# Kernel optimization log

Hardware: AMD Instinct MI355X
Metric: run time of the kernel (lower is better)

## Reference

```python
import jax, jax.numpy as jnp
import numpy as np
from jax import lax

TOP_N = 4
CAT_NUM = 4
IOU_THRESH = 0.25
PAD = 224
OUT_SZ = 224


def _gen_edge_anchors():
    # Faithful port of NTSNet._generate_default_anchor_maps for 448x448 input.
    settings = (
        dict(stride=32, size=48, scale=[2 ** (1.0 / 3.0), 2 ** (2.0 / 3.0)], ar=[0.667, 1, 1.5]),
        dict(stride=64, size=96, scale=[2 ** (1.0 / 3.0), 2 ** (2.0 / 3.0)], ar=[0.667, 1, 1.5]),
        dict(stride=128, size=192, scale=[1, 2 ** (1.0 / 3.0), 2 ** (2.0 / 3.0)], ar=[0.667, 1, 1.5]),
    )
    inp = np.array([448, 448], dtype=np.float32)
    edges = []
    for s in settings:
        stride = s['stride']
        oh, ow = np.ceil(inp / stride).astype(int)
        ostart = stride / 2.0
        oy = np.arange(ostart, ostart + stride * oh, stride, dtype=np.float32).reshape(oh, 1)
        ox = np.arange(ostart, ostart + stride * ow, stride, dtype=np.float32).reshape(1, ow)
        cy = np.broadcast_to(oy, (oh, ow)); cx = np.broadcast_to(ox, (oh, ow))
        for sc in s['scale']:
            for ar in s['ar']:
                h = s['size'] * sc / float(ar) ** 0.5
                w = s['size'] * sc * float(ar) ** 0.5
                e = np.stack([cy - h / 2.0, cx - w / 2.0, cy + h / 2.0, cx + w / 2.0], axis=-1).reshape(-1, 4)
                edges.append(e)
    return np.concatenate(edges, 0).astype(np.float32)

EDGE_ANCHORS = (_gen_edge_anchors() + PAD).astype(np.int32)  # [1614,4] (y0,x0,y1,x1) in padded coords
BOXES_F = jnp.asarray(EDGE_ANCHORS, jnp.float32)
BOXES_I = jnp.asarray(EDGE_ANCHORS, jnp.int32)
AREAS = (BOXES_F[:, 2] - BOXES_F[:, 0]) * (BOXES_F[:, 3] - BOXES_F[:, 1])
N_ANCHORS = EDGE_ANCHORS.shape[0]  # 1614


def _nms_single(scores):
    # Greedy hard NMS: pick top score, suppress IoU >= thresh, repeat TOP_N times.
    def step(valid, _):
        s = jnp.where(valid, scores, -jnp.inf)
        i = jnp.argmax(s)
        b = BOXES_F[i]
        sy = jnp.maximum(BOXES_F[:, 0], b[0]); sx = jnp.maximum(BOXES_F[:, 1], b[1])
        ey = jnp.minimum(BOXES_F[:, 2], b[2]); ex = jnp.minimum(BOXES_F[:, 3], b[3])
        ly = ey - sy; lx = ex - sx
        inter = jnp.where((ly < 0) | (lx < 0), 0.0, ly * lx)
        iou = inter / (AREAS + AREAS[i] - inter)
        return valid & (iou < IOU_THRESH), i
    _, idx = lax.scan(step, jnp.ones((N_ANCHORS,), bool), None, length=TOP_N)
    return idx  # [TOP_N] int


def _crop_resize(img, box):
    # img: [3, 896, 896]; box: int [4] = (y0,x0,y1,x1); bilinear, align_corners=True -> [3,224,224]
    hmax = img.shape[-1] - 1
    y0, x0, y1, x1 = box[0], box[1], box[2], box[3]
    t = jnp.arange(OUT_SZ, dtype=jnp.float32) / (OUT_SZ - 1.0)
    ys = y0.astype(jnp.float32) + t * (y1 - y0 - 1).astype(jnp.float32)
    xs = x0.astype(jnp.float32) + t * (x1 - x0 - 1).astype(jnp.float32)
    yf = jnp.floor(ys); xf = jnp.floor(xs)
    wy = (ys - yf)[None, :, None]; wx = (xs - xf)[None, None, :]
    yl = yf.astype(jnp.int32); yh = jnp.minimum(yl + 1, hmax)
    xl = xf.astype(jnp.int32); xh = jnp.minimum(xl + 1, hmax)
    g = lambda yi, xi: img[:, yi[:, None], xi[None, :]]
    top = g(yl, xl) * (1.0 - wx) + g(yl, xh) * wx
    bot = g(yh, xl) * (1.0 - wx) + g(yh, xh) * wx
    return top * (1.0 - wy) + bot * wy


def _conv(x, w, b, stride, pad):
    y = lax.conv_general_dilated(x, w, (stride, stride), ((pad, pad), (pad, pad)),
                                 dimension_numbers=('NCHW', 'OIHW', 'NCHW'))
    return y + b[None, :, None, None]


def _forward(x, bb_w, bb_b, w1, b1, t1w, t1b, w2, b2, t2w, t2b, w3, b3, t3w, t3b, cw, cb):
    B = x.shape[0]
    backbone = lambda z: jax.nn.relu(_conv(z, bb_w, bb_b, 32, 0))
    raw_pre = backbone(x)  # [B,2048,14,14]
    # Navigator unit
    y1 = jax.nn.relu(_conv(raw_pre, w1, b1, 1, 1))                                  # [B,128,14,14]
    z1 = (jnp.einsum('bchw,oc->bohw', y1, t1w) + t1b[None, :, None, None]).reshape(B, -1)
    y2 = jax.nn.relu(_conv(y1, w2, b2, 2, 1))                                        # [B,128,7,7]
    z2 = (jnp.einsum('bchw,oc->bohw', y2, t2w) + t2b[None, :, None, None]).reshape(B, -1)
    y3 = jax.nn.relu(_conv(y2, w3, b3, 2, 1))                                        # [B,128,4,4]
    z3 = (jnp.einsum('bchw,oc->bohw', y3, t3w) + t3b[None, :, None, None]).reshape(B, -1)
    rpn_score = jnp.concatenate([z1, z2, z3], axis=1)  # [B,1614]
    top_idx = jax.vmap(_nms_single)(rpn_score)          # [B,TOP_N]
    boxes = BOXES_I[top_idx]                            # [B,TOP_N,4]
    x_pad = jnp.pad(x, ((0, 0), (0, 0), (PAD, PAD), (PAD, PAD)))  # [B,3,896,896]
    parts = jax.vmap(lambda img, bs: jax.vmap(lambda b: _crop_resize(img, b))(bs))(x_pad, boxes)
    parts = lax.stop_gradient(parts).reshape(B * TOP_N, 3, OUT_SZ, OUT_SZ)  # .detach() in torch
    part_feat = backbone(parts).mean(axis=(2, 3)).reshape(B, TOP_N, 2048)
    part_feat = part_feat[:, :CAT_NUM].reshape(B, -1)   # [B,8192]
    raw_feat = lax.stop_gradient(raw_pre).mean(axis=(2, 3))  # [B,2048] (detached in torch)
    concat = jnp.concatenate([part_feat, raw_feat], axis=1)  # [B,10240]
    return concat @ cw.T + cb                           # [B,200]


def setup_inputs() -> dict:
    key = jax.random.key(0)
    ks = jax.random.split(key, 12)
    def w(k, shape, fan_in):
        return jax.random.normal(k, shape, jnp.float32) * np.float32(np.sqrt(2.0 / fan_in))
    return {
        'x': jax.random.normal(ks[0], (8, 3, 448, 448), jnp.float32),
        'bb_w': w(ks[1], (2048, 3, 32, 32), 3 * 32 * 32), 'bb_b': jnp.zeros((2048,), jnp.float32),
        'w1': w(ks[2], (128, 2048, 3, 3), 2048 * 9), 'b1': jnp.zeros((128,), jnp.float32),
        't1w': w(ks[3], (6, 128), 128), 't1b': jnp.zeros((6,), jnp.float32),
        'w2': w(ks[4], (128, 128, 3, 3), 128 * 9), 'b2': jnp.zeros((128,), jnp.float32),
        't2w': w(ks[5], (6, 128), 128), 't2b': jnp.zeros((6,), jnp.float32),
        'w3': w(ks[6], (128, 128, 3, 3), 128 * 9), 'b3': jnp.zeros((128,), jnp.float32),
        't3w': w(ks[7], (9, 128), 128), 't3b': jnp.zeros((9,), jnp.float32),
        'cw': w(ks[8], (200, 2048 * (CAT_NUM + 1)), 2048 * (CAT_NUM + 1)),
        'cb': jnp.zeros((200,), jnp.float32),
    }


def reference(x, bb_w, bb_b, w1, b1, t1w, t1b, w2, b2, t2w, t2b, w3, b3, t3w, t3b, cw, cb):
    return _forward(x, bb_w, bb_b, w1, b1, t1w, t1b, w2, b2, t2w, t2b, w3, b3, t3w, t3b, cw, cb)
```

## Files before the change

kernel.cpp:

```cpp
#include <hip/hip_runtime.h>
#include <math.h>


typedef _Float16 h8 __attribute__((ext_vector_type(8)));
typedef float f32x4 __attribute__((ext_vector_type(4)));

#define ASCALE 256.0f
#define WSCALE 16384.0f
#define RSCALE (1.0f / (256.0f * 16384.0f))
#define PSLAB ((size_t)1664 * 2048)

__device__ __forceinline__ void gload16(const void* g, void* l) {
  __builtin_amdgcn_global_load_lds(
      (__attribute__((address_space(1))) void*)(void*)(uintptr_t)g,
      (__attribute__((address_space(3))) void*)l, 16, 0, 0);
}

__device__ void anchors_body(int i, int* anch, float* areas) {
  if (i >= 1614) return;
  int stride, oh, a, pos;
  double size, sc;
  const double C13 = 1.2599210498948732;
  const double C23 = 1.5874010519681994;
  if (i < 1176) {
    stride = 32; size = 48.0; oh = 14; a = i / 196; pos = i % 196;
    sc = (a / 3 == 0) ? C13 : C23;
  } else if (i < 1470) {
    int r = i - 1176; stride = 64; size = 96.0; oh = 7; a = r / 49; pos = r % 49;
    sc = (a / 3 == 0) ? C13 : C23;
  } else {
    int r = i - 1470; stride = 128; size = 192.0; oh = 4; a = r / 16; pos = r % 16;
    int si = a / 3;
    sc = (si == 0) ? 1.0 : ((si == 1) ? C13 : C23);
  }
  int ari = a % 3;
  double ar = (ari == 0) ? 0.667 : ((ari == 1) ? 1.0 : 1.5);
  int gy = pos / oh, gx = pos % oh;
  float cy = 0.5f * (float)stride + (float)(stride * gy);
  float cx = 0.5f * (float)stride + (float)(stride * gx);
  double ss = sqrt(ar);
  double hd = (size * sc) / ss;
  double wd = (size * sc) * ss;
  float hh = (float)(hd * 0.5), wh = (float)(wd * 0.5);
  int y0 = (int)((cy - hh) + 224.0f), x0 = (int)((cx - wh) + 224.0f);
  int y1i = (int)((cy + hh) + 224.0f), x1i = (int)((cx + wh) + 224.0f);
  anch[i * 4 + 0] = y0; anch[i * 4 + 1] = x0;
  anch[i * 4 + 2] = y1i; anch[i * 4 + 3] = x1i;
  areas[i] = (float)(y1i - y0) * (float)(x1i - x0);
}

__global__ __launch_bounds__(256) void prep_small(int* __restrict__ anch,
                                                  float* __restrict__ areas,
                                                  const float* __restrict__ w2,
                                                  float* __restrict__ w2p,
                                                  const float* __restrict__ w3,
                                                  float* __restrict__ w3p) {
  int b = blockIdx.x, t = threadIdx.x;
  if (b < 7) { anchors_body(b * 256 + t, anch, areas); return; }
  const float* src; float* dst; int idx;
  if (b < 7 + 576) { src = w2; dst = w2p; idx = (b - 7) * 256 + t; }
  else             { src = w3; dst = w3p; idx = (b - 583) * 256 + t; }
  if (idx >= 128 * 9 * 128) return;
  int c = idx % 128; int r2 = idx / 128; int tap = r2 % 9; int o = r2 / 9;
  dst[idx] = src[(o * 128 + c) * 9 + tap];
}

__global__ __launch_bounds__(256) void split_w(const float* __restrict__ src,
                                               _Float16* __restrict__ h,
                                               _Float16* __restrict__ l, int n8) {
  int i = blockIdx.x * 256 + threadIdx.x;
  if (i >= n8) return;
  float4 v0 = *(const float4*)(src + (size_t)i * 8);
  float4 v1 = *(const float4*)(src + (size_t)i * 8 + 4);
  float vv[8] = {v0.x, v0.y, v0.z, v0.w, v1.x, v1.y, v1.z, v1.w};
  h8 vh, vl;
#pragma unroll
  for (int j = 0; j < 8; ++j) {
    float s = vv[j] * WSCALE;
    _Float16 a = (_Float16)s;
    vh[j] = a; vl[j] = (_Float16)(s - (float)a);
  }
  *(h8*)(h + (size_t)i * 8) = vh;
  *(h8*)(l + (size_t)i * 8) = vl;
}

__global__ __launch_bounds__(256) void split_w1(const float* __restrict__ w1,
                                                _Float16* __restrict__ h,
                                                _Float16* __restrict__ l) {
  int idx = blockIdx.x * 256 + threadIdx.x;
  if (idx >= 128 * 9 * 2048) return;
  int c = idx & 2047; int rest = idx >> 11; int tap = rest % 9; int o = rest / 9;
  float v = w1[(o * 2048 + c) * 9 + tap] * WSCALE;
  _Float16 a = (_Float16)v;
  h[idx] = a; l[idx] = (_Float16)(v - (float)a);
}

__global__ __launch_bounds__(256) void split_x(const float* __restrict__ x,
                                               _Float16* __restrict__ Ah,
                                               _Float16* __restrict__ Al) {
  int i = blockIdx.x * 256 + threadIdx.x;
  if (i >= 1664 * 384) return;
  int kq = i % 384, m = i / 384;
  int k = kq * 8;
  h8 vh = {}, vl = {};
  if (m < 1568) {
    int b = m / 196, pos = m % 196;
    int c = k >> 10, r = (k >> 5) & 31, col = k & 31;
    int py = (pos / 14) * 32 + r, px = (pos % 14) * 32 + col;
    const float* sp2 = x + (((size_t)(b * 3 + c) * 448 + py) * 448 + px);
    float4 v0 = *(const float4*)sp2;
    float4 v1 = *(const float4*)(sp2 + 4);
    float vv[8] = {v0.x, v0.y, v0.z, v0.w, v1.x, v1.y, v1.z, v1.w};
#pragma unroll
    for (int j = 0; j < 8; ++j) {
      float s = vv[j] * ASCALE;
      _Float16 a = (_Float16)s;
      vh[j] = a; vl[j] = (_Float16)(s - (float)a);
    }
  }
  *(h8*)(Ah + (size_t)m * 3072 + k) = vh;
  *(h8*)(Al + (size_t)m * 3072 + k) = vl;
}

__global__ __launch_bounds__(256) void gemm_bb_mfma(
    const _Float16* __restrict__ Ah, const _Float16* __restrict__ Al,
    const _Float16* __restrict__ Bh, const _Float16* __restrict__ Bl,
    float* __restrict__ P) {
  __shared__ __align__(16) char lds[65536];
  const int t = threadIdx.x;
  const int bid = blockIdx.x + 13 * blockIdx.y;
  const int orig = (bid & 7) * 26 + (bid >> 3);
  const int m0 = (orig % 13) * 128, n0 = (orig / 13) * 128;
  const int kz = blockIdx.z;
  const int lane = t & 63, w = t >> 6;
  const int wm = (w >> 1) * 64, wn = (w & 1) * 64;
  const int lrow = lane & 15, kg = lane >> 4;

  int offA[4], offB[4];
#pragma unroll
  for (int i = 0; i < 4; ++i) {
    int ba = (wm + i * 16 + lrow) * 64 + kg * 16;
    offA[i] = ba ^ (((ba >> 7) & 3) << 4);
    int bb2 = (wn + i * 16 + lrow) * 64 + kg * 16;
    offB[i] = bb2 ^ (((bb2 >> 7) & 3) << 4);
  }
  size_t gAo[2], gBo[2];
  int ldso[2];
#pragma unroll
  for (int e = 0; e < 2; ++e) {
    int p = e * 256 + t;
    int lsl = p ^ ((p >> 3) & 3);
    int row = lsl >> 2, kq = lsl & 3;
    gAo[e] = (size_t)(m0 + row) * 3072 + kq * 8;
    gBo[e] = (size_t)(n0 + row) * 3072 + kq * 8;
    ldso[e] = e * 4096 + (t & 192) * 16;
  }

  auto STAGE = [&](int buf, int k0) {
    char* L = lds + buf * 32768;
#pragma unroll
    for (int e = 0; e < 2; ++e) {
      gload16(Ah + gAo[e] + k0, L + ldso[e]);
      gload16(Al + gAo[e] + k0, L + 8192 + ldso[e]);
      gload16(Bh + gBo[e] + k0, L + 16384 + ldso[e]);
      gload16(Bl + gBo[e] + k0, L + 24576 + ldso[e]);
    }
  };

  f32x4 acc[4][4] = {};
  const int kbeg = kz * 1536, kend = kbeg + 1536;
  STAGE(0, kbeg);
  __syncthreads();
  int cur = 0;
  for (int k0 = kbeg; k0 < kend; k0 += 32) {
    if (k0 + 32 < kend) STAGE(cur ^ 1, k0 + 32);
    const char* L = lds + cur * 32768;
    h8 fah[4], fal[4], fbh[4], fbl[4];
#pragma unroll
    for (int i = 0; i < 4; ++i) {
      fah[i] = *(const h8*)(L + offA[i]);
      fal[i] = *(const h8*)(L + 8192 + offA[i]);
      fbh[i] = *(const h8*)(L + 16384 + offB[i]);
      fbl[i] = *(const h8*)(L + 24576 + offB[i]);
    }
#pragma unroll
    for (int i = 0; i < 4; ++i)
#pragma unroll
      for (int j = 0; j < 4; ++j)
        acc[i][j] = __builtin_amdgcn_mfma_f32_16x16x32_f16(fah[i], fbh[j], acc[i][j], 0, 0, 0);
#pragma unroll
    for (int i = 0; i < 4; ++i)
#pragma unroll
      for (int j = 0; j < 4; ++j)
        acc[i][j] = __builtin_amdgcn_mfma_f32_16x16x32_f16(fah[i], fbl[j], acc[i][j], 0, 0, 0);
#pragma unroll
    for (int i = 0; i < 4; ++i)
#pragma unroll
      for (int j = 0; j < 4; ++j)
        acc[i][j] = __builtin_amdgcn_mfma_f32_16x16x32_f16(fal[i], fbh[j], acc[i][j], 0, 0, 0);
    __syncthreads();
    cur ^= 1;
  }
  float* Pz = P + (size_t)kz * PSLAB;
  const int prow = (lane >> 4) * 4;
#pragma unroll
  for (int i = 0; i < 4; ++i) {
#pragma unroll
    for (int j = 0; j < 4; ++j) {
      int n = n0 + wn + j * 16 + lrow;
#pragma unroll
      for (int r = 0; r < 4; ++r) {
        int m = m0 + wm + i * 16 + prow + r;
        Pz[(size_t)m * 2048 + n] = acc[i][j][r];
      }
    }
  }
}

__global__ __launch_bounds__(256) void bb_reduce_split(const float* __restrict__ P,
                                                       const float* __restrict__ bias,
                                                       _Float16* __restrict__ h,
                                                       _Float16* __restrict__ l) {
  int idx = blockIdx.x * 256 + threadIdx.x;
  int m = idx >> 8, col = (idx & 255) * 8;
  if (m >= 1664) return;
  size_t o = (size_t)m * 2048 + col;
  if (m >= 1568) {
    h8 z = {};
    *(h8*)(h + o) = z;
    *(h8*)(l + o) = z;
    return;
  }
  h8 vh, vl;
#pragma unroll
  for (int q = 0; q < 2; ++q) {
    float4 s0 = *(const float4*)(P + o + q * 4);
    float4 s1 = *(const float4*)(P + PSLAB + o + q * 4);
    float4 b = *(const float4*)(bias + col + q * 4);
    float v[4];
    v[0] = fmaxf(fmaf(s0.x + s1.x, RSCALE, b.x), 0.f);
    v[1] = fmaxf(fmaf(s0.y + s1.y, RSCALE, b.y), 0.f);
    v[2] = fmaxf(fmaf(s0.z + s1.z, RSCALE, b.z), 0.f);
    v[3] = fmaxf(fmaf(s0.w + s1.w, RSCALE, b.w), 0.f);
#pragma unroll
    for (int j = 0; j < 4; ++j) {
      float s = v[j] * ASCALE;
      _Float16 a = (_Float16)s;
      vh[q * 4 + j] = a; vl[q * 4 + j] = (_Float16)(s - (float)a);
    }
  }
  *(h8*)(h + o) = vh;
  *(h8*)(l + o) = vl;
}

__global__ __launch_bounds__(256) void feat_reduce(const float* __restrict__ P,
                                                   const float* __restrict__ bias,
                                                   float* __restrict__ out,
                                                   int rows) {
  int g = blockIdx.x >> 5, chunk = blockIdx.x & 31;
  int col = chunk * 64 + (threadIdx.x & 63), rl = threadIdx.x >> 6;
  const float* base0 = P + ((size_t)g * rows) * 2048 + col;
  const float* base1 = base0 + PSLAB;
  float bcol = bias[col];
  float s = 0.f;
  for (int r = rl; r < rows; r += 4)
    s += fmaxf(fmaf(base0[(size_t)r * 2048] + base1[(size_t)r * 2048], RSCALE, bcol), 0.f);
  __shared__ float red[4][64];
  red[rl][threadIdx.x & 63] = s;
  __syncthreads();
  if (rl == 0) {
    int c = threadIdx.x & 63;
    out[(size_t)g * 2048 + col] =
        ((red[0][c] + red[1][c]) + (red[2][c] + red[3][c])) / (float)rows;
  }
}

__global__ __launch_bounds__(256) void gemm_nav_mfma(
    const _Float16* __restrict__ Ah, const _Float16* __restrict__ Al,
    const _Float16* __restrict__ Bh, const _Float16* __restrict__ Bl,
    float* __restrict__ part) {
  __shared__ __align__(16) char lds[65536];
  const int t = threadIdx.x;
  const int bid = blockIdx.x + 13 * blockIdx.y;
  const int orig = (bid & 7) * 52 + (bid >> 3);
  const int m0 = (orig % 13) * 128;
  const int sp = orig / 13;
  const int lane = t & 63, w = t >> 6;
  const int wm = (w >> 1) * 64, wn = (w & 1) * 64;
  const int lrow = lane & 15, kg = lane >> 4;

  int offA[4], offB[4];
#pragma unroll
  for (int i = 0; i < 4; ++i) {
    int ba = (wm + i * 16 + lrow) * 64 + kg * 16;
    offA[i] = ba ^ (((ba >> 7) & 3) << 4);
    int bb2 = (wn + i * 16 + lrow) * 64 + kg * 16;
    offB[i] = bb2 ^ (((bb2 >> 7) & 3) << 4);
  }
  size_t gBo[2];
  int ldso[2], akq8[2], ab[2], apy[2], apx[2], amv[2];
#pragma unroll
  for (int e = 0; e < 2; ++e) {
    int p = e * 256 + t;
    int lsl = p ^ ((p >> 3) & 3);
    int row = lsl >> 2, kq = lsl & 3;
    gBo[e] = (size_t)row * 18432 + kq * 8;
    ldso[e] = e * 4096 + (t & 192) * 16;
    int m = m0 + row;
    amv[e] = (m < 1568);
    int b = m / 196, pos = m % 196;
    ab[e] = b; apy[e] = pos / 14; apx[e] = pos % 14;
    akq8[e] = kq * 8;
  }

  auto STAGE = [&](int buf, int k0) {
    const int tap = k0 >> 11;
    const int c = k0 & 2047;
    const int dy = tap / 3 - 1, dx = tap % 3 - 1;
    char* L = lds + buf * 32768;
#pragma unroll
    for (int e = 0; e < 2; ++e) {
      int sy = apy[e] + dy, sx = apx[e] + dx;
      bool ok = amv[e] && ((unsigned)sy < 14u) && ((unsigned)sx < 14u);
      size_t rowi = ok ? (size_t)(ab[e] * 196 + sy * 14 + sx) : (size_t)1600;
      size_t ao = rowi * 2048 + c + akq8[e];
      gload16(Ah + ao, L + ldso[e]);
      gload16(Al + ao, L + 8192 + ldso[e]);
      gload16(Bh + gBo[e] + k0, L + 16384 + ldso[e]);
      gload16(Bl + gBo[e] + k0, L + 24576 + ldso[e]);
    }
  };

  f32x4 acc[4][4] = {};
  const int kbeg = sp * 576, kend = kbeg + 576;
  STAGE(0, kbeg);
  __syncthreads();
  int cur = 0;
  for (int k0 = kbeg; k0 < kend; k0 += 32) {
    if (k0 + 32 < kend) STAGE(cur ^ 1, k0 + 32);
    const char* L = lds + cur * 32768;
    h8 fah[4], fal[4], fbh[4], fbl[4];
#pragma unroll
    for (int i = 0; i < 4; ++i) {
      fah[i] = *(const h8*)(L + offA[i]);
      fal[i] = *(const h8*)(L + 8192 + offA[i]);
      fbh[i] = *(const h8*)(L + 16384 + offB[i]);
      fbl[i] = *(const h8*)(L + 24576 + offB[i]);
    }
#pragma unroll
    for (int i = 0; i < 4; ++i)
#pragma unroll
      for (int j = 0; j < 4; ++j)
        acc[i][j] = __builtin_amdgcn_mfma_f32_16x16x32_f16(fah[i], fbh[j], acc[i][j], 0, 0, 0);
#pragma unroll
    for (int i = 0; i < 4; ++i)
#pragma unroll
      for (int j = 0; j < 4; ++j)
        acc[i][j] = __builtin_amdgcn_mfma_f32_16x16x32_f16(fah[i], fbl[j], acc[i][j], 0, 0, 0);
#pragma unroll
    for (int i = 0; i < 4; ++i)
#pragma unroll
      for (int j = 0; j < 4; ++j)
        acc[i][j] = __builtin_amdgcn_mfma_f32_16x16x32_f16(fal[i], fbh[j], acc[i][j], 0, 0, 0);
    __syncthreads();
    cur ^= 1;
  }
  const int prow = (lane >> 4) * 4;
#pragma unroll
  for (int i = 0; i < 4; ++i) {
#pragma unroll
    for (int j = 0; j < 4; ++j) {
      int n = wn + j * 16 + lrow;
#pragma unroll
      for (int r = 0; r < 4; ++r) {
        int m = m0 + wm + i * 16 + prow + r;
        if (m < 1568)
          part[((size_t)sp * 1568 + m) * 128 + n] = acc[i][j][r] * RSCALE;
      }
    }
  }
}

__global__ __launch_bounds__(256) void y1_reduce(const float* __restrict__ part,
                                                 const float* __restrict__ b1,
                                                 float* __restrict__ y1) {
  int idx = blockIdx.x * 256 + threadIdx.x;
  if (idx >= 1568 * 128) return;
  int o = idx & 127;
  float s = b1[o];
#pragma unroll
  for (int sp = 0; sp < 32; ++sp) s += part[(size_t)sp * 1568 * 128 + idx];
  y1[idx] = fmaxf(s, 0.f);
}

__global__ __launch_bounds__(256) void conv3x3s2(const float* __restrict__ in,
                                                 const float* __restrict__ wp,
                                                 const float* __restrict__ bias,
                                                 float* __restrict__ out,
                                                 int Hin, int Hout) {
  int idx = blockIdx.x * 256 + threadIdx.x;
  int total = 8 * Hout * Hout * 128;
  if (idx >= total) return;
  int o = idx & 127; int pos = idx >> 7;
  int ox = pos % Hout; int t2 = pos / Hout; int oy = t2 % Hout; int b = t2 / Hout;
  float acc = bias[o];
  for (int dy = 0; dy < 3; ++dy) {
    int iy = 2 * oy - 1 + dy;
    if (iy < 0 || iy >= Hin) continue;
    for (int dx = 0; dx < 3; ++dx) {
      int ix = 2 * ox - 1 + dx;
      if (ix < 0 || ix >= Hin) continue;
      const float* ip = in + ((b * Hin + iy) * Hin + ix) * 128;
      const float* wgt = wp + (o * 9 + dy * 3 + dx) * 128;
#pragma unroll 4
      for (int c = 0; c < 128; c += 4) {
        float4 a = *(const float4*)(ip + c);
        float4 ww = *(const float4*)(wgt + c);
        acc += a.x * ww.x + a.y * ww.y + a.z * ww.z + a.w * ww.w;
      }
    }
  }
  out[idx] = fmaxf(acc, 0.f);
}

__global__ __launch_bounds__(256) void scores_kernel(
    const float* __restrict__ y1, const float* __restrict__ y2,
    const float* __restrict__ y3, const float* __restrict__ t1w,
    const float* __restrict__ t1b, const float* __restrict__ t2w,
    const float* __restrict__ t2b, const float* __restrict__ t3w,
    const float* __restrict__ t3b, float* __restrict__ scores) {
  int idx = blockIdx.x * 256 + threadIdx.x;
  if (idx >= 8 * 1614) return;
  int b = idx / 1614, sI = idx % 1614;
  const float* f; const float* w; float bias;
  if (sI < 1176) {
    int a = sI / 196;
    f = y1 + (b * 196 + (sI % 196)) * 128; w = t1w + a * 128; bias = t1b[a];
  } else if (sI < 1470) {
    int r = sI - 1176; int a = r / 49;
    f = y2 + (b * 49 + (r % 49)) * 128; w = t2w + a * 128; bias = t2b[a];
  } else {
    int r = sI - 1470; int a = r / 16;
    f = y3 + (b * 16 + (r % 16)) * 128; w = t3w + a * 128; bias = t3b[a];
  }
  float acc = 0.f;
  for (int c = 0; c < 128; c += 4) {
    float4 a4 = *(const float4*)(f + c);
    float4 w4 = *(const float4*)(w + c);
    acc += a4.x * w4.x + a4.y * w4.y + a4.z * w4.z + a4.w * w4.w;
  }
  scores[idx] = acc + bias;
}

__global__ __launch_bounds__(256) void nms_kernel(const float* __restrict__ scores,
                                                  const int* __restrict__ anch,
                                                  const float* __restrict__ areas,
                                                  int* __restrict__ boxes) {
  const int b = blockIdx.x, t = threadIdx.x;
  const float* s = scores + b * 1614;
  __shared__ unsigned char valid[1614];
  __shared__ float rv[256];
  __shared__ int ri[256];
  for (int i = t; i < 1614; i += 256) valid[i] = 1;
  __syncthreads();
  for (int n = 0; n < 4; ++n) {
    float best = -INFINITY; int bi = 0x7fffffff;
    for (int i = t; i < 1614; i += 256) {
      if (valid[i]) {
        float v = s[i];
        if (v > best || (v == best && i < bi)) { best = v; bi = i; }
      }
    }
    rv[t] = best; ri[t] = bi;
    __syncthreads();
    for (int off = 128; off > 0; off >>= 1) {
      if (t < off) {
        float ov = rv[t + off]; int oi = ri[t + off];
        if (ov > rv[t] || (ov == rv[t] && oi < ri[t])) { rv[t] = ov; ri[t] = oi; }
      }
      __syncthreads();
    }
    int sel = ri[0];
    if (sel > 1613) sel = 0;
    const int4 bb = ((const int4*)anch)[sel];
    const float Ai = areas[sel];
    if (t == 0) ((int4*)boxes)[b * 4 + n] = bb;
    __syncthreads();
    for (int i = t; i < 1614; i += 256) {
      if (!valid[i]) continue;
      const int4 ab = ((const int4*)anch)[i];
      float sy = fmaxf((float)ab.x, (float)bb.x);
      float sx = fmaxf((float)ab.y, (float)bb.y);
      float ey = fminf((float)ab.z, (float)bb.z);
      float ex = fminf((float)ab.w, (float)bb.w);
      float ly = ey - sy, lx = ex - sx;
      float inter = (ly < 0.f || lx < 0.f) ? 0.f : ly * lx;
      float iou = inter / (areas[i] + Ai - inter);
      if (iou >= 0.25f) valid[i] = 0;
    }
    __syncthreads();
  }
}

__global__ __launch_bounds__(256) void crop_kernel(const float* __restrict__ x,
                                                   const int* __restrict__ boxes,
                                                   _Float16* __restrict__ Ah,
                                                   _Float16* __restrict__ Al) {
  int idx = blockIdx.x * 256 + threadIdx.x;
  if (idx >= 32 * 3 * 224 * 224) return;
  int px = idx % 224; int t1 = idx / 224; int py = t1 % 224; int t2 = t1 / 224;
  int c = t2 % 3; int p = t2 / 3;
  int b = p >> 2;
  const int4 bb = ((const int4*)boxes)[p];
  float ty = (float)py / 223.0f;
  float txf = (float)px / 223.0f;
  float ys = (float)bb.x + ty * (float)(bb.z - bb.x - 1);
  float xs = (float)bb.y + txf * (float)(bb.w - bb.y - 1);
  float yf = floorf(ys), xf = floorf(xs);
  float wy = ys - yf, wx = xs - xf;
  int yl = (int)yf, xl = (int)xf;
  int yh = min(yl + 1, 895), xh = min(xl + 1, 895);
  const float* img = x + (size_t)(b * 3 + c) * 448 * 448;
  auto samp = [&](int yy, int xx) -> float {
    yy -= 224; xx -= 224;
    if (yy < 0 || yy >= 448 || xx < 0 || xx >= 448) return 0.f;
    return img[yy * 448 + xx];
  };
  float v00 = samp(yl, xl), v01 = samp(yl, xh);
  float v10 = samp(yh, xl), v11 = samp(yh, xh);
  float top = v00 * (1.f - wx) + v01 * wx;
  float bot = v10 * (1.f - wx) + v11 * wx;
  float val = top * (1.f - wy) + bot * wy;
  int i = py >> 5, r = py & 31, j = px >> 5, col = px & 31;
  int m = p * 49 + i * 7 + j;
  int k = (c << 10) + (r << 5) + col;
  float s = val * ASCALE;
  _Float16 a = (_Float16)s;
  Ah[(size_t)m * 3072 + k] = a;
  Al[(size_t)m * 3072 + k] = (_Float16)(s - (float)a);
}

__global__ __launch_bounds__(256) void final_kernel(const float* __restrict__ pfeat,
                                                    const float* __restrict__ rfeat,
                                                    const float* __restrict__ cw,
                                                    const float* __restrict__ cb,
                                                    float* __restrict__ out) {
  int gw = (blockIdx.x * 256 + threadIdx.x) >> 6;
  int lane = threadIdx.x & 63;
  if (gw >= 1600) return;
  int b = gw / 200, j = gw % 200;
  const float* wr = cw + (size_t)j * 10240;
  const float* pf = pfeat + (size_t)b * 8192;
  float acc = 0.f;
  for (int k = lane * 4; k < 8192; k += 256) {
    float4 a = *(const float4*)(pf + k);
    float4 w = *(const float4*)(wr + k);
    acc += a.x * w.x + a.y * w.y + a.z * w.z + a.w * w.w;
  }
  const float* rf = rfeat + (size_t)b * 2048;
  const float* wr2 = wr + 8192;
  for (int k = lane * 4; k < 2048; k += 256) {
    float4 a = *(const float4*)(rf + k);
    float4 w = *(const float4*)(wr2 + k);
    acc += a.x * w.x + a.y * w.y + a.z * w.z + a.w * w.w;
  }
#pragma unroll
  for (int off = 32; off > 0; off >>= 1) acc += __shfl_down(acc, off, 64);
  if (lane == 0) out[b * 200 + j] = acc + cb[j];
}

extern "C" void kernel_launch(void* const* d_in, const int* in_sizes, int n_in,
                              void* d_out, int out_size, void* d_ws, size_t ws_size,
                              hipStream_t stream) {
  const float* x   = (const float*)d_in[0];
  const float* bbw = (const float*)d_in[1];
  const float* bbb = (const float*)d_in[2];
  const float* w1  = (const float*)d_in[3];
  const float* b1  = (const float*)d_in[4];
  const float* t1w = (const float*)d_in[5];
  const float* t1b = (const float*)d_in[6];
  const float* w2  = (const float*)d_in[7];
  const float* b2  = (const float*)d_in[8];
  const float* t2w = (const float*)d_in[9];
  const float* t2b = (const float*)d_in[10];
  const float* w3  = (const float*)d_in[11];
  const float* b3  = (const float*)d_in[12];
  const float* t3w = (const float*)d_in[13];
  const float* t3b = (const float*)d_in[14];
  const float* cw  = (const float*)d_in[15];
  const float* cb  = (const float*)d_in[16];
  float* out = (float*)d_out;

  char* p = (char*)d_ws;
  auto alloc = [&](size_t bytes) -> char* {
    char* r = p; p += (bytes + 255) & ~(size_t)255; return r;
  };
  int*      anch  = (int*)     alloc((size_t)1614 * 4 * 4);
  float*    areas = (float*)   alloc((size_t)1614 * 4);
  _Float16* bWh   = (_Float16*)alloc((size_t)2048 * 3072 * 2);
  _Float16* bWl   = (_Float16*)alloc((size_t)2048 * 3072 * 2);
  _Float16* w1h   = (_Float16*)alloc((size_t)128 * 18432 * 2);
  _Float16* w1l   = (_Float16*)alloc((size_t)128 * 18432 * 2);
  _Float16* Ahh   = (_Float16*)alloc((size_t)1664 * 3072 * 2);
  _Float16* All   = (_Float16*)alloc((size_t)1664 * 3072 * 2);
  _Float16* rawh  = (_Float16*)alloc((size_t)1664 * 2048 * 2);
  _Float16* rawl  = (_Float16*)alloc((size_t)1664 * 2048 * 2);
  float*    w2p   = (float*)   alloc((size_t)128 * 9 * 128 * 4);
  float*    w3p   = (float*)   alloc((size_t)128 * 9 * 128 * 4);
  char*     big   = alloc((size_t)2 * PSLAB * 4);
  float*    Pbuf  = (float*)big;
  float*    y1s   = (float*)big;
  float*    y1v   = (float*)   alloc((size_t)1568 * 128 * 4);
  float*    y2v   = (float*)   alloc((size_t)392 * 128 * 4);
  float*    y3v   = (float*)   alloc((size_t)128 * 128 * 4);
  float*    sc    = (float*)   alloc((size_t)8 * 1614 * 4);
  int*      boxes = (int*)     alloc((size_t)8 * 4 * 4 * 4);
  float*    pfeat = (float*)   alloc((size_t)32 * 2048 * 4);
  float*    rfeat = (float*)   alloc((size_t)8 * 2048 * 4);

  prep_small<<<7 + 576 + 576, 256, 0, stream>>>(anch, areas, w2, w2p, w3, w3p);
  split_w<<<(2048 * 3072 / 8 + 255) / 256, 256, 0, stream>>>(bbw, bWh, bWl, 2048 * 3072 / 8);
  split_w1<<<(128 * 9 * 2048 + 255) / 256, 256, 0, stream>>>(w1, w1h, w1l);
  split_x<<<(1664 * 384 + 255) / 256, 256, 0, stream>>>(x, Ahh, All);

  gemm_bb_mfma<<<dim3(13, 16, 2), 256, 0, stream>>>(Ahh, All, bWh, bWl, Pbuf);
  bb_reduce_split<<<1664, 256, 0, stream>>>(Pbuf, bbb, rawh, rawl);
  feat_reduce<<<8 * 32, 256, 0, stream>>>(Pbuf, bbb, rfeat, 196);
  gemm_nav_mfma<<<dim3(13, 32), 256, 0, stream>>>(rawh, rawl, w1h, w1l, y1s);
  y1_reduce<<<(1568 * 128 + 255) / 256, 256, 0, stream>>>(y1s, b1, y1v);
  conv3x3s2<<<(8 * 7 * 7 * 128 + 255) / 256, 256, 0, stream>>>(y1v, w2p, b2, y2v, 14, 7);
  conv3x3s2<<<(8 * 4 * 4 * 128 + 255) / 256, 256, 0, stream>>>(y2v, w3p, b3, y3v, 7, 4);
  scores_kernel<<<(8 * 1614 + 255) / 256, 256, 0, stream>>>(
      y1v, y2v, y3v, t1w, t1b, t2w, t2b, t3w, t3b, sc);
  nms_kernel<<<8, 256, 0, stream>>>(sc, anch, areas, boxes);
  crop_kernel<<<(32 * 3 * 224 * 224) / 256, 256, 0, stream>>>(x, boxes, Ahh, All);
  gemm_bb_mfma<<<dim3(13, 16, 2), 256, 0, stream>>>(Ahh, All, bWh, bWl, Pbuf);
  feat_reduce<<<32 * 32, 256, 0, stream>>>(Pbuf, bbb, pfeat, 49);
  final_kernel<<<400, 256, 0, stream>>>(pfeat, rfeat, cw, cb, out);
}
```

Measured before the change: 372.9 us.

## Vectorize small kernels, transpose w1 via LDS, wave-shuffle NMS, remap GEMM tiles

The w1 split now stages a slab in LDS so the transpose from o,c,tap to o,tap,c reads global memory coalesced. y1_reduce and crop_kernel now handle 4 and 8 elements per thread with vector loads and stores. NMS argmax uses wave shuffles instead of an LDS tree with many barriers. The backbone GEMM block-to-tile mapping is changed to a new swizzle, which alters L2 reuse and may help or hurt.

```diff
diff --git a/kernel.cpp b/kernel.cpp
--- a/kernel.cpp
+++ b/kernel.cpp
@@ -87,12 +87,18 @@
 __global__ __launch_bounds__(256) void split_w1(const float* __restrict__ w1,
                                                 _Float16* __restrict__ h,
                                                 _Float16* __restrict__ l) {
-  int idx = blockIdx.x * 256 + threadIdx.x;
-  if (idx >= 128 * 9 * 2048) return;
-  int c = idx & 2047; int rest = idx >> 11; int tap = rest % 9; int o = rest / 9;
-  float v = w1[(o * 2048 + c) * 9 + tap] * WSCALE;
-  _Float16 a = (_Float16)v;
-  h[idx] = a; l[idx] = (_Float16)(v - (float)a);
+  __shared__ float buf[4608];
+  int o = blockIdx.x >> 2, ct = (blockIdx.x & 3) * 512;
+  const float* src = w1 + (size_t)o * 18432 + (size_t)ct * 9;
+  for (int i = threadIdx.x; i < 4608; i += 256) buf[i] = src[i];
+  __syncthreads();
+  for (int i = threadIdx.x; i < 4608; i += 256) {
+    int tap = i / 512, c = i - tap * 512;
+    float v = buf[c * 9 + tap] * WSCALE;
+    _Float16 a = (_Float16)v;
+    size_t o2 = ((size_t)o * 9 + tap) * 2048 + ct + c;
+    h[o2] = a; l[o2] = (_Float16)(v - (float)a);
+  }
 }
 
 __global__ __launch_bounds__(256) void split_x(const float* __restrict__ x,
@@ -129,8 +135,9 @@
   __shared__ __align__(16) char lds[65536];
   const int t = threadIdx.x;
   const int bid = blockIdx.x + 13 * blockIdx.y;
-  const int orig = (bid & 7) * 26 + (bid >> 3);
-  const int m0 = (orig % 13) * 128, n0 = (orig / 13) * 128;
+  const int r = bid >> 3;
+  const int m0 = (r >> 1) * 128;
+  const int n0 = ((bid & 7) * 2 + (r & 1)) * 128;
   const int kz = blockIdx.z;
   const int lane = t & 63, w = t >> 6;
   const int wm = (w >> 1) * 64, wn = (w & 1) * 64;
@@ -209,9 +216,9 @@
     for (int j = 0; j < 4; ++j) {
       int n = n0 + wn + j * 16 + lrow;
 #pragma unroll
-      for (int r = 0; r < 4; ++r) {
-        int m = m0 + wm + i * 16 + prow + r;
-        Pz[(size_t)m * 2048 + n] = acc[i][j][r];
+      for (int r2 = 0; r2 < 4; ++r2) {
+        int m = m0 + wm + i * 16 + prow + r2;
+        Pz[(size_t)m * 2048 + n] = acc[i][j][r2];
       }
     }
   }
@@ -385,12 +392,17 @@
                                                  const float* __restrict__ b1,
                                                  float* __restrict__ y1) {
   int idx = blockIdx.x * 256 + threadIdx.x;
-  if (idx >= 1568 * 128) return;
-  int o = idx & 127;
-  float s = b1[o];
-#pragma unroll
-  for (int sp = 0; sp < 32; ++sp) s += part[(size_t)sp * 1568 * 128 + idx];
-  y1[idx] = fmaxf(s, 0.f);
+  if (idx >= 1568 * 32) return;
+  int o = (idx * 4) & 127;
+  float4 s = *(const float4*)(b1 + o);
+#pragma unroll
+  for (int sp = 0; sp < 32; ++sp) {
+    float4 v = *(const float4*)(part + (size_t)sp * 1568 * 128 + (size_t)idx * 4);
+    s.x += v.x; s.y += v.y; s.z += v.z; s.w += v.w;
+  }
+  s.x = fmaxf(s.x, 0.f); s.y = fmaxf(s.y, 0.f);
+  s.z = fmaxf(s.z, 0.f); s.w = fmaxf(s.w, 0.f);
+  *(float4*)(y1 + (size_t)idx * 4) = s;
 }
 
 __global__ __launch_bounds__(256) void conv3x3s2(const float* __restrict__ in,
@@ -457,10 +469,12 @@
                                                   const float* __restrict__ areas,
                                                   int* __restrict__ boxes) {
   const int b = blockIdx.x, t = threadIdx.x;
+  const int lane = t & 63, wid = t >> 6;
   const float* s = scores + b * 1614;
   __shared__ unsigned char valid[1614];
-  __shared__ float rv[256];
-  __shared__ int ri[256];
+  __shared__ float wv[4];
+  __shared__ int wi[4];
+  __shared__ int ssel;
   for (int i = t; i < 1614; i += 256) valid[i] = 1;
   __syncthreads();
   for (int n = 0; n < 4; ++n) {
@@ -471,21 +485,27 @@
         if (v > best || (v == best && i < bi)) { best = v; bi = i; }
       }
     }
-    rv[t] = best; ri[t] = bi;
+#pragma unroll
+    for (int off = 32; off > 0; off >>= 1) {
+      float ov = __shfl_down(best, off, 64);
+      int oi = __shfl_down(bi, off, 64);
+      if (ov > best || (ov == best && oi < bi)) { best = ov; bi = oi; }
+    }
+    if (lane == 0) { wv[wid] = best; wi[wid] = bi; }
     __syncthreads();
-    for (int off = 128; off > 0; off >>= 1) {
-      if (t < off) {
-        float ov = rv[t + off]; int oi = ri[t + off];
-        if (ov > rv[t] || (ov == rv[t] && oi < ri[t])) { rv[t] = ov; ri[t] = oi; }
-      }
-      __syncthreads();
-    }
-    int sel = ri[0];
-    if (sel > 1613) sel = 0;
+    if (t == 0) {
+      float bv = wv[0]; int bj = wi[0];
+#pragma unroll
+      for (int q = 1; q < 4; ++q)
+        if (wv[q] > bv || (wv[q] == bv && wi[q] < bj)) { bv = wv[q]; bj = wi[q]; }
+      if (bj > 1613) bj = 0;
+      ssel = bj;
+      ((int4*)boxes)[b * 4 + n] = ((const int4*)anch)[bj];
+    }
+    __syncthreads();
+    int sel = ssel;
     const int4 bb = ((const int4*)anch)[sel];
     const float Ai = areas[sel];
-    if (t == 0) ((int4*)boxes)[b * 4 + n] = bb;
-    __syncthreads();
     for (int i = t; i < 1614; i += 256) {
       if (!valid[i]) continue;
       const int4 ab = ((const int4*)anch)[i];
@@ -507,37 +527,48 @@
                                                    _Float16* __restrict__ Ah,
                                                    _Float16* __restrict__ Al) {
   int idx = blockIdx.x * 256 + threadIdx.x;
-  if (idx >= 32 * 3 * 224 * 224) return;
-  int px = idx % 224; int t1 = idx / 224; int py = t1 % 224; int t2 = t1 / 224;
+  if (idx >= 32 * 3 * 224 * 28) return;
+  int pxq = idx % 28; int t1 = idx / 28; int py = t1 % 224; int t2 = t1 / 224;
   int c = t2 % 3; int p = t2 / 3;
   int b = p >> 2;
+  int px0 = pxq * 8;
   const int4 bb = ((const int4*)boxes)[p];
   float ty = (float)py / 223.0f;
-  float txf = (float)px / 223.0f;
   float ys = (float)bb.x + ty * (float)(bb.z - bb.x - 1);
-  float xs = (float)bb.y + txf * (float)(bb.w - bb.y - 1);
-  float yf = floorf(ys), xf = floorf(xs);
-  float wy = ys - yf, wx = xs - xf;
-  int yl = (int)yf, xl = (int)xf;
-  int yh = min(yl + 1, 895), xh = min(xl + 1, 895);
+  float yf = floorf(ys);
+  float wy = ys - yf;
+  int yl = (int)yf;
+  int yh = min(yl + 1, 895);
   const float* img = x + (size_t)(b * 3 + c) * 448 * 448;
   auto samp = [&](int yy, int xx) -> float {
     yy -= 224; xx -= 224;
     if (yy < 0 || yy >= 448 || xx < 0 || xx >= 448) return 0.f;
     return img[yy * 448 + xx];
   };
-  float v00 = samp(yl, xl), v01 = samp(yl, xh);
-  float v10 = samp(yh, xl), v11 = samp(yh, xh);
-  float top = v00 * (1.f - wx) + v01 * wx;
-  float bot = v10 * (1.f - wx) + v11 * wx;
-  float val = top * (1.f - wy) + bot * wy;
-  int i = py >> 5, r = py & 31, j = px >> 5, col = px & 31;
+  h8 vh, vl;
+#pragma unroll
+  for (int q = 0; q < 8; ++q) {
+    int px = px0 + q;
+    float txf = (float)px / 223.0f;
+    float xs = (float)bb.y + txf * (float)(bb.w - bb.y - 1);
+    float xf = floorf(xs);
+    float wx = xs - xf;
+    int xl = (int)xf;
+    int xh = min(xl + 1, 895);
+    float v00 = samp(yl, xl), v01 = samp(yl, xh);
+    float v10 = samp(yh, xl), v11 = samp(yh, xh);
+    float top = v00 * (1.f - wx) + v01 * wx;
+    float bot = v10 * (1.f - wx) + v11 * wx;
+    float val = top * (1.f - wy) + bot * wy;
+    float sv = val * ASCALE;
+    _Float16 a = (_Float16)sv;
+    vh[q] = a; vl[q] = (_Float16)(sv - (float)a);
+  }
+  int i = py >> 5, r = py & 31, j = px0 >> 5, col = px0 & 31;
   int m = p * 49 + i * 7 + j;
   int k = (c << 10) + (r << 5) + col;
-  float s = val * ASCALE;
-  _Float16 a = (_Float16)s;
-  Ah[(size_t)m * 3072 + k] = a;
-  Al[(size_t)m * 3072 + k] = (_Float16)(s - (float)a);
+  *(h8*)(Ah + (size_t)m * 3072 + k) = vh;
+  *(h8*)(Al + (size_t)m * 3072 + k) = vl;
 }
 
 __global__ __launch_bounds__(256) void final_kernel(const float* __restrict__ pfeat,
@@ -620,20 +651,20 @@
 
   prep_small<<<7 + 576 + 576, 256, 0, stream>>>(anch, areas, w2, w2p, w3, w3p);
   split_w<<<(2048 * 3072 / 8 + 255) / 256, 256, 0, stream>>>(bbw, bWh, bWl, 2048 * 3072 / 8);
-  split_w1<<<(128 * 9 * 2048 + 255) / 256, 256, 0, stream>>>(w1, w1h, w1l);
+  split_w1<<<512, 256, 0, stream>>>(w1, w1h, w1l);
   split_x<<<(1664 * 384 + 255) / 256, 256, 0, stream>>>(x, Ahh, All);
 
   gemm_bb_mfma<<<dim3(13, 16, 2), 256, 0, stream>>>(Ahh, All, bWh, bWl, Pbuf);
   bb_reduce_split<<<1664, 256, 0, stream>>>(Pbuf, bbb, rawh, rawl);
   feat_reduce<<<8 * 32, 256, 0, stream>>>(Pbuf, bbb, rfeat, 196);
   gemm_nav_mfma<<<dim3(13, 32), 256, 0, stream>>>(rawh, rawl, w1h, w1l, y1s);
-  y1_reduce<<<(1568 * 128 + 255) / 256, 256, 0, stream>>>(y1s, b1, y1v);
+  y1_reduce<<<(1568 * 32 + 255) / 256, 256, 0, stream>>>(y1s, b1, y1v);
   conv3x3s2<<<(8 * 7 * 7 * 128 + 255) / 256, 256, 0, stream>>>(y1v, w2p, b2, y2v, 14, 7);
   conv3x3s2<<<(8 * 4 * 4 * 128 + 255) / 256, 256, 0, stream>>>(y2v, w3p, b3, y3v, 7, 4);
   scores_kernel<<<(8 * 1614 + 255) / 256, 256, 0, stream>>>(
       y1v, y2v, y3v, t1w, t1b, t2w, t2b, t3w, t3b, sc);
   nms_kernel<<<8, 256, 0, stream>>>(sc, anch, areas, boxes);
-  crop_kernel<<<(32 * 3 * 224 * 224) / 256, 256, 0, stream>>>(x, boxes, Ahh, All);
+  crop_kernel<<<(32 * 3 * 224 * 28 + 255) / 256, 256, 0, stream>>>(x, boxes, Ahh, All);
   gemm_bb_mfma<<<dim3(13, 16, 2), 256, 0, stream>>>(Ahh, All, bWh, bWl, Pbuf);
   feat_reduce<<<32 * 32, 256, 0, stream>>>(Pbuf, bbb, pfeat, 49);
   final_kernel<<<400, 256, 0, stream>>>(pfeat, rfeat, cw, cb, out);
```

Result: no change. 371.8 us (-0.3%).
